# Kernel tuning notes

Measured on AMD Instinct MI355X. Metric: run time of the kernel, lower is better.

The kernel has to match this reference:

```python
import jax, jax.numpy as jnp
import numpy as np

T, H, E, K, I = 2048, 2048, 64, 8, 768
CAP = 512


def setup_inputs() -> dict:
    key = jax.random.key(0)
    ks = jax.random.split(key, 5)
    s = 0.02
    return {
        "hidden_states": jax.random.normal(ks[0], (T, H), jnp.float32),
        "w_router": jax.random.normal(ks[1], (E, H), jnp.float32) * s,
        "w_gate": jax.random.normal(ks[2], (E, H, I), jnp.float32) * s,
        "w_up": jax.random.normal(ks[3], (E, H, I), jnp.float32) * s,
        "w_down": jax.random.normal(ks[4], (E, I, H), jnp.float32) * s,
    }


def _moe(x, w_router, w_gate, w_up, w_down):
    Tn = x.shape[0]
    # --- router: softmax -> top-k -> renormalize (norm_topk_prob=True) ---
    logits = x @ w_router.T                                   # [T, E]
    probs = jax.nn.softmax(logits.astype(jnp.float32), axis=-1)
    topk_w, topk_idx = jax.lax.top_k(probs, K)                # [T, K]
    topk_w = topk_w / jnp.sum(topk_w, axis=-1, keepdims=True)
    # --- dispatch: sort (token, expert) pairs by expert, scatter into capacity buffers ---
    e = topk_idx.reshape(-1)                                  # [T*K] expert id per pair
    t = jnp.repeat(jnp.arange(Tn), K)                         # [T*K] token id per pair
    w = topk_w.reshape(-1)                                    # [T*K] combine weight per pair
    order = jnp.argsort(e, stable=True)
    e_s, t_s, w_s = e[order], t[order], w[order]
    counts = jax.ops.segment_sum(jnp.ones_like(e_s), e_s, num_segments=E)  # [E]
    starts = jnp.cumsum(counts) - counts                      # start offset of each expert group
    pos = jnp.arange(Tn * K) - starts[e_s]                    # slot within expert
    valid = pos < CAP
    posc = jnp.where(valid, pos, 0)
    vm = valid.astype(x.dtype)[:, None]
    buf = jnp.zeros((E, CAP, H), x.dtype).at[e_s, posc].add(x[t_s] * vm)   # [E, C, H]
    # --- grouped expert SwiGLU FFN: down(silu(gate(x)) * up(x)) ---
    g = jnp.einsum('ech,ehi->eci', buf, w_gate)               # [E, C, I]
    u = jnp.einsum('ech,ehi->eci', buf, w_up)                 # [E, C, I]
    y = jnp.einsum('eci,eih->ech', jax.nn.silu(g) * u, w_down)  # [E, C, H]
    # --- combine: gather expert outputs back to tokens, weighted sum ---
    gw = (w_s.astype(x.dtype) * valid.astype(x.dtype))[:, None]
    out = jnp.zeros((Tn, H), x.dtype).at[t_s].add(gw * y[e_s, posc])
    return out


def reference(hidden_states, w_router, w_gate, w_up, w_down):
    return _moe(hidden_states, w_router, w_gate, w_up, w_down)
```

## Files before the change

### kernel.cpp

```cpp
#include <hip/hip_runtime.h>
#include <hip/hip_bf16.h>
#include <math.h>

#define T_TOK 2048
#define H_DIM 2048
#define NEXP  64
#define TOPK  8
#define I_DIM 768
#define CAPE  512
#define MTMAX 4
#define LDW   40

typedef short bf16x8 __attribute__((ext_vector_type(8)));
typedef short bf16x4 __attribute__((ext_vector_type(4)));
typedef float f32x4  __attribute__((ext_vector_type(4)));

__device__ __forceinline__ unsigned short f2bf(float f) {
  unsigned u = __float_as_uint(f);
  u += 0x7fffu + ((u >> 16) & 1u);
  return (unsigned short)(u >> 16);
}
__device__ __forceinline__ float bf2f(unsigned short b) {
  return __uint_as_float(((unsigned)b) << 16);
}
__device__ __forceinline__ unsigned pack2(float lo, float hi) {
  return (unsigned)f2bf(lo) | ((unsigned)f2bf(hi) << 16);
}

__global__ __launch_bounds__(256) void k_router(const float* __restrict__ x,
                                                const float* __restrict__ wr,
                                                int* __restrict__ topk_idx,
                                                float* __restrict__ topk_w) {
  const int lane = threadIdx.x & 63;
  const int t = blockIdx.x * 4 + (threadIdx.x >> 6);
  const float4* xr   = (const float4*)(x + (size_t)t * H_DIM);
  const float4* wrow = (const float4*)(wr + (size_t)lane * H_DIM);
  double acc = 0.0;
  for (int i = 0; i < H_DIM / 4; ++i) {
    float4 a = xr[i], b = wrow[i];
    acc += (double)a.x * b.x; acc += (double)a.y * b.y;
    acc += (double)a.z * b.z; acc += (double)a.w * b.w;
  }
  float cur = (float)acc;
  float val[TOPK]; int idx[TOPK];
#pragma unroll
  for (int r = 0; r < TOPK; ++r) {
    float bv = cur; int bi = lane;
#pragma unroll
    for (int off = 32; off > 0; off >>= 1) {
      float ov = __shfl_xor(bv, off);
      int   oi = __shfl_xor(bi, off);
      if (ov > bv || (ov == bv && oi < bi)) { bv = ov; bi = oi; }
    }
    val[r] = bv; idx[r] = bi;
    if (lane == bi) cur = -INFINITY;
  }
  float m = val[0], s = 0.f, w[TOPK];
#pragma unroll
  for (int r = 0; r < TOPK; ++r) { w[r] = expf(val[r] - m); s += w[r]; }
  if (lane < TOPK) {
    topk_idx[t * TOPK + lane] = idx[lane];
    topk_w [t * TOPK + lane] = w[lane] / s;
  }
}

__global__ __launch_bounds__(256) void k_rank(const int* __restrict__ topk_idx,
                                              int* __restrict__ pair_pos,
                                              int* __restrict__ slot_token,
                                              int* __restrict__ cnts) {
  __shared__ int s_run[64];
  __shared__ int s_whist[4][64];
  const int tid = threadIdx.x, lane = tid & 63, wv = tid >> 6;
  if (tid < 64) s_run[tid] = 0;
  for (int c = 0; c < 64; ++c) {
    const int p = c * 256 + tid;
    const int e = topk_idx[p];
    __syncthreads();
    s_whist[wv][lane] = 0;
    __syncthreads();
    unsigned long long m = ~0ull;
#pragma unroll
    for (int b = 0; b < 6; ++b) {
      unsigned long long bb = __ballot((e >> b) & 1);
      m &= ((e >> b) & 1) ? bb : ~bb;
    }
    const int rw = __popcll(m & ((1ull << lane) - 1ull));
    if (rw == 0) s_whist[wv][e] = __popcll(m);
    __syncthreads();
    int r = rw;
    for (int w2 = 0; w2 < wv; ++w2) r += s_whist[w2][e];
    const int pos = s_run[e] + r;
    pair_pos[p] = pos;
    if (pos < CAPE) slot_token[e * CAPE + pos] = p >> 3;
    __syncthreads();
    if (tid < 64)
      s_run[tid] += s_whist[0][tid] + s_whist[1][tid] + s_whist[2][tid] + s_whist[3][tid];
  }
  __syncthreads();
  if (tid < 64) cnts[tid] = s_run[tid];
}

__global__ __launch_bounds__(512) void k_gateup(const float* __restrict__ x,
                                                const float* __restrict__ wg,
                                                const float* __restrict__ wu,
                                                const int* __restrict__ slot_token,
                                                const int* __restrict__ cnts,
                                                unsigned short* __restrict__ act) {
  const int NB = NEXP * MTMAX * 6;
  const int v = (blockIdx.x & 7) * (NB / 8) + (blockIdx.x >> 3);
  const int e = v / (MTMAX * 6);
  const int rem = v % (MTMAX * 6);
  const int mt = rem / 6, nt = rem % 6;

  int cnt = cnts[e]; cnt = cnt < CAPE ? cnt : CAPE;
  if (cnt <= 0 || mt * 128 >= cnt) return;
  const int m0 = mt << 7;

  __shared__ __align__(16) short As[2][128 * LDW];
  __shared__ __align__(16) short Bg[2][128 * LDW];
  __shared__ __align__(16) short Bu[2][128 * LDW];

  const int tid = threadIdx.x;
  const int lane = tid & 63, wave = tid >> 6;
  const int wm = wave >> 2, wn = wave & 3;
  const int lr = lane & 15, lg = lane >> 4;

  const int a_row0 = tid >> 3, a_kq = tid & 7;
  const int a_row1 = a_row0 + 64;
  const int b_kp = tid & 15, b_nq = tid >> 4;
  const int bk = 2 * b_kp, bn = 4 * b_nq;
  const size_t wbase = (size_t)e * H_DIM * I_DIM + (size_t)nt * 128;

  const int tok0 = (m0 + a_row0 < cnt) ? slot_token[e * CAPE + m0 + a_row0] : 0;
  const int tok1 = (m0 + a_row1 < cnt) ? slot_token[e * CAPE + m0 + a_row1] : 0;
  const float* xr0 = x + (size_t)tok0 * H_DIM + a_kq * 4;
  const float* xr1 = x + (size_t)tok1 * H_DIM + a_kq * 4;
  const float* gp  = wg + wbase + (size_t)bk * I_DIM + bn;
  const float* up  = wu + wbase + (size_t)bk * I_DIM + bn;

  f32x4 accg[4][2], accu[4][2];
#pragma unroll
  for (int mi = 0; mi < 4; ++mi)
#pragma unroll
    for (int ni = 0; ni < 2; ++ni) {
      accg[mi][ni] = (f32x4){0.f, 0.f, 0.f, 0.f};
      accu[mi][ni] = (f32x4){0.f, 0.f, 0.f, 0.f};
    }

  struct Tile { float4 a0, a1, g0, g1, u0, u1; };

  auto LOAD = [&](Tile& Tl, int kt) {
    const int k0 = kt * 32;
    Tl.a0 = *(const float4*)(xr0 + k0);
    Tl.a1 = *(const float4*)(xr1 + k0);
    Tl.g0 = *(const float4*)(gp + (size_t)k0 * I_DIM);
    Tl.g1 = *(const float4*)(gp + (size_t)k0 * I_DIM + I_DIM);
    Tl.u0 = *(const float4*)(up + (size_t)k0 * I_DIM);
    Tl.u1 = *(const float4*)(up + (size_t)k0 * I_DIM + I_DIM);
  };
  auto STORE = [&](const Tile& Tl, int b) {
    bf16x4 s0, s1;
    s0[0]=(short)f2bf(Tl.a0.x); s0[1]=(short)f2bf(Tl.a0.y); s0[2]=(short)f2bf(Tl.a0.z); s0[3]=(short)f2bf(Tl.a0.w);
    s1[0]=(short)f2bf(Tl.a1.x); s1[1]=(short)f2bf(Tl.a1.y); s1[2]=(short)f2bf(Tl.a1.z); s1[3]=(short)f2bf(Tl.a1.w);
    *(bf16x4*)(&As[b][a_row0 * LDW + a_kq * 4]) = s0;
    *(bf16x4*)(&As[b][a_row1 * LDW + a_kq * 4]) = s1;
    *(unsigned*)(&Bg[b][(bn + 0) * LDW + bk]) = pack2(Tl.g0.x, Tl.g1.x);
    *(unsigned*)(&Bg[b][(bn + 1) * LDW + bk]) = pack2(Tl.g0.y, Tl.g1.y);
    *(unsigned*)(&Bg[b][(bn + 2) * LDW + bk]) = pack2(Tl.g0.z, Tl.g1.z);
    *(unsigned*)(&Bg[b][(bn + 3) * LDW + bk]) = pack2(Tl.g0.w, Tl.g1.w);
    *(unsigned*)(&Bu[b][(bn + 0) * LDW + bk]) = pack2(Tl.u0.x, Tl.u1.x);
    *(unsigned*)(&Bu[b][(bn + 1) * LDW + bk]) = pack2(Tl.u0.y, Tl.u1.y);
    *(unsigned*)(&Bu[b][(bn + 2) * LDW + bk]) = pack2(Tl.u0.z, Tl.u1.z);
    *(unsigned*)(&Bu[b][(bn + 3) * LDW + bk]) = pack2(Tl.u0.w, Tl.u1.w);
  };
  auto COMPUTE = [&](int b) {
    bf16x8 a[4], bg[2], bu[2];
#pragma unroll
    for (int mi = 0; mi < 4; ++mi)
      a[mi] = *(const bf16x8*)(&As[b][(wm * 64 + mi * 16 + lr) * LDW + lg * 8]);
#pragma unroll
    for (int ni = 0; ni < 2; ++ni) {
      bg[ni] = *(const bf16x8*)(&Bg[b][(wn * 32 + ni * 16 + lr) * LDW + lg * 8]);
      bu[ni] = *(const bf16x8*)(&Bu[b][(wn * 32 + ni * 16 + lr) * LDW + lg * 8]);
    }
#pragma unroll
    for (int mi = 0; mi < 4; ++mi)
#pragma unroll
      for (int ni = 0; ni < 2; ++ni) {
        accg[mi][ni] = __builtin_amdgcn_mfma_f32_16x16x32_bf16(a[mi], bg[ni], accg[mi][ni], 0, 0, 0);
        accu[mi][ni] = __builtin_amdgcn_mfma_f32_16x16x32_bf16(a[mi], bu[ni], accu[mi][ni], 0, 0, 0);
      }
  };

  const int NK = H_DIM / 32;
  Tile tA, tB;
  LOAD(tA, 0);
  STORE(tA, 0);
  LOAD(tB, 1);
  __syncthreads();

  int t = 0;
#pragma unroll 1
  for (; t + 2 < NK; t += 2) {
    LOAD(tA, t + 2);
    COMPUTE(0);
    STORE(tB, 1);
    __syncthreads();
    LOAD(tB, t + 3);
    COMPUTE(1);
    STORE(tA, 0);
    __syncthreads();
  }
  COMPUTE(0);
  STORE(tB, 1);
  __syncthreads();
  COMPUTE(1);

#pragma unroll
  for (int mi = 0; mi < 4; ++mi)
#pragma unroll
    for (int ni = 0; ni < 2; ++ni)
#pragma unroll
      for (int r = 0; r < 4; ++r) {
        const int row = m0 + wm * 64 + mi * 16 + lg * 4 + r;
        const int col = nt * 128 + wn * 32 + ni * 16 + lr;
        const float g = accg[mi][ni][r], u = accu[mi][ni][r];
        const float vv = (g / (1.f + __expf(-g))) * u;
        act[(size_t)(e * CAPE + row) * I_DIM + col] = f2bf(vv);
      }
}

__global__ __launch_bounds__(512) void k_down(const unsigned short* __restrict__ act,
                                              const float* __restrict__ wd,
                                              const int* __restrict__ cnts,
                                              unsigned short* __restrict__ y) {
  const int NB = NEXP * MTMAX * 16;
  const int v = (blockIdx.x & 7) * (NB / 8) + (blockIdx.x >> 3);
  const int e = v / (MTMAX * 16);
  const int rem = v % (MTMAX * 16);
  const int mt = rem / 16, nt = rem % 16;

  int cnt = cnts[e]; cnt = cnt < CAPE ? cnt : CAPE;
  if (cnt <= 0 || mt * 128 >= cnt) return;
  const int m0 = mt << 7;

  __shared__ __align__(16) short As[2][128 * LDW];
  __shared__ __align__(16) short Bt[2][128 * LDW];

  const int tid = threadIdx.x;
  const int lane = tid & 63, wave = tid >> 6;
  const int wm = wave >> 2, wn = wave & 3;
  const int lr = lane & 15, lg = lane >> 4;

  const int a_row = tid >> 2, a_ko = (tid & 3) * 8;
  const int b_kp = tid & 15, b_nq = tid >> 4;
  const int bk = 2 * b_kp, bn = 4 * b_nq;
  const size_t wbase = (size_t)e * I_DIM * H_DIM + (size_t)nt * 128;

  const unsigned short* ap = act + (size_t)(e * CAPE + m0 + a_row) * I_DIM + a_ko;
  const float* dp = wd + wbase + (size_t)bk * H_DIM + bn;

  f32x4 acc[4][2];
#pragma unroll
  for (int mi = 0; mi < 4; ++mi)
#pragma unroll
    for (int ni = 0; ni < 2; ++ni) acc[mi][ni] = (f32x4){0.f, 0.f, 0.f, 0.f};

  struct Tile { bf16x8 a; float4 d0, d1; };

  auto LOAD = [&](Tile& Tl, int kt) {
    const int k0 = kt * 32;
    Tl.a  = *(const bf16x8*)(ap + k0);
    Tl.d0 = *(const float4*)(dp + (size_t)k0 * H_DIM);
    Tl.d1 = *(const float4*)(dp + (size_t)k0 * H_DIM + H_DIM);
  };
  auto STORE = [&](const Tile& Tl, int b) {
    *(bf16x8*)(&As[b][a_row * LDW + a_ko]) = Tl.a;
    *(unsigned*)(&Bt[b][(bn + 0) * LDW + bk]) = pack2(Tl.d0.x, Tl.d1.x);
    *(unsigned*)(&Bt[b][(bn + 1) * LDW + bk]) = pack2(Tl.d0.y, Tl.d1.y);
    *(unsigned*)(&Bt[b][(bn + 2) * LDW + bk]) = pack2(Tl.d0.z, Tl.d1.z);
    *(unsigned*)(&Bt[b][(bn + 3) * LDW + bk]) = pack2(Tl.d0.w, Tl.d1.w);
  };
  auto COMPUTE = [&](int b) {
    bf16x8 a[4], bb[2];
#pragma unroll
    for (int mi = 0; mi < 4; ++mi)
      a[mi] = *(const bf16x8*)(&As[b][(wm * 64 + mi * 16 + lr) * LDW + lg * 8]);
#pragma unroll
    for (int ni = 0; ni < 2; ++ni)
      bb[ni] = *(const bf16x8*)(&Bt[b][(wn * 32 + ni * 16 + lr) * LDW + lg * 8]);
#pragma unroll
    for (int mi = 0; mi < 4; ++mi)
#pragma unroll
      for (int ni = 0; ni < 2; ++ni)
        acc[mi][ni] = __builtin_amdgcn_mfma_f32_16x16x32_bf16(a[mi], bb[ni], acc[mi][ni], 0, 0, 0);
  };

  const int NK = I_DIM / 32;
  Tile tA, tB;
  LOAD(tA, 0);
  STORE(tA, 0);
  LOAD(tB, 1);
  __syncthreads();

  int t = 0;
#pragma unroll 1
  for (; t + 2 < NK; t += 2) {
    LOAD(tA, t + 2);
    COMPUTE(0);
    STORE(tB, 1);
    __syncthreads();
    LOAD(tB, t + 3);
    COMPUTE(1);
    STORE(tA, 0);
    __syncthreads();
  }
  COMPUTE(0);
  STORE(tB, 1);
  __syncthreads();
  COMPUTE(1);

#pragma unroll
  for (int mi = 0; mi < 4; ++mi)
#pragma unroll
    for (int ni = 0; ni < 2; ++ni)
#pragma unroll
      for (int r = 0; r < 4; ++r) {
        const int row = m0 + wm * 64 + mi * 16 + lg * 4 + r;
        const int col = nt * 128 + wn * 32 + ni * 16 + lr;
        y[(size_t)(e * CAPE + row) * H_DIM + col] = f2bf(acc[mi][ni][r]);
      }
}

__global__ __launch_bounds__(256) void k_combine(const unsigned short* __restrict__ y,
                                                 const int* __restrict__ topk_idx,
                                                 const float* __restrict__ topk_w,
                                                 const int* __restrict__ pair_pos,
                                                 float* __restrict__ out) {
  const int t = blockIdx.x;
  __shared__ int s_e[TOPK]; __shared__ int s_p[TOPK]; __shared__ float s_w[TOPK];
  if (threadIdx.x < TOPK) {
    s_e[threadIdx.x] = topk_idx[t * TOPK + threadIdx.x];
    s_p[threadIdx.x] = pair_pos[t * TOPK + threadIdx.x];
    s_w[threadIdx.x] = topk_w [t * TOPK + threadIdx.x];
  }
  __syncthreads();
  const int h0 = threadIdx.x * 8;
  float acc[8] = {0.f, 0.f, 0.f, 0.f, 0.f, 0.f, 0.f, 0.f};
#pragma unroll
  for (int k = 0; k < TOPK; ++k) {
    const int pos = s_p[k];
    if (pos >= CAPE) continue;
    const float w = s_w[k];
    const bf16x8 vv = *(const bf16x8*)(&y[(size_t)(s_e[k] * CAPE + pos) * H_DIM + h0]);
#pragma unroll
    for (int j = 0; j < 8; ++j) acc[j] += w * bf2f((unsigned short)vv[j]);
  }
  float4 o0 = {acc[0], acc[1], acc[2], acc[3]};
  float4 o1 = {acc[4], acc[5], acc[6], acc[7]};
  *(float4*)(out + (size_t)t * H_DIM + h0)     = o0;
  *(float4*)(out + (size_t)t * H_DIM + h0 + 4) = o1;
}

extern "C" void kernel_launch(void* const* d_in, const int* in_sizes, int n_in,
                              void* d_out, int out_size, void* d_ws, size_t ws_size,
                              hipStream_t stream) {
  const float* x   = (const float*)d_in[0];
  const float* wr  = (const float*)d_in[1];
  const float* wgt = (const float*)d_in[2];
  const float* wup = (const float*)d_in[3];
  const float* wdn = (const float*)d_in[4];
  float* out = (float*)d_out;

  char* ws = (char*)d_ws;
  int*            topk_idx   = (int*)(ws);
  float*          topk_w     = (float*)(ws + 65536);
  int*            pair_pos   = (int*)(ws + 131072);
  int*            cnts       = (int*)(ws + 196608);
  int*            slot_token = (int*)(ws + 196864);
  unsigned short* act        = (unsigned short*)(ws + 327936);
  unsigned short* yb         = (unsigned short*)(ws + 327936 + 50331648);

  k_router <<<dim3(T_TOK / 4),        dim3(256), 0, stream>>>(x, wr, topk_idx, topk_w);
  k_rank   <<<dim3(1),                dim3(256), 0, stream>>>(topk_idx, pair_pos, slot_token, cnts);
  k_gateup <<<dim3(NEXP * MTMAX * 6), dim3(512), 0, stream>>>(x, wgt, wup, slot_token, cnts, act);
  k_down   <<<dim3(NEXP * MTMAX * 16),dim3(512), 0, stream>>>(act, wdn, cnts, yb);
  k_combine<<<dim3(T_TOK),            dim3(256), 0, stream>>>(yb, topk_idx, topk_w, pair_pos, out);
}
```

Before: 803.6 us.

## Fuse combine into down-projection epilogue with weighted atomic adds to output

The down-projection kernel now scales each output row by its routing weight and atomically adds it straight into the token's output row. This removes the bf16 intermediate y buffer and the separate combine kernel. The rank kernel now records per-slot weights, and the output is zeroed with a memset. The bf16 packing also switches to the hardware paired-conversion intrinsic. The cost is many fp32 atomics to global memory (8 per output element) and a summation order that is no longer deterministic.

```diff
diff --git a/kernel.cpp b/kernel.cpp
--- a/kernel.cpp
+++ b/kernel.cpp
@@ -24,7 +24,8 @@
   return __uint_as_float(((unsigned)b) << 16);
 }
 __device__ __forceinline__ unsigned pack2(float lo, float hi) {
-  return (unsigned)f2bf(lo) | ((unsigned)f2bf(hi) << 16);
+  __hip_bfloat162 h = __float22bfloat162_rn(make_float2(lo, hi));
+  unsigned r; __builtin_memcpy(&r, &h, 4); return r;
 }
 
 __global__ __launch_bounds__(256) void k_router(const float* __restrict__ x,
@@ -65,8 +66,9 @@
 }
 
 __global__ __launch_bounds__(256) void k_rank(const int* __restrict__ topk_idx,
-                                              int* __restrict__ pair_pos,
+                                              const float* __restrict__ topk_w,
                                               int* __restrict__ slot_token,
+                                              float* __restrict__ slot_w,
                                               int* __restrict__ cnts) {
   __shared__ int s_run[64];
   __shared__ int s_whist[4][64];
@@ -90,8 +92,10 @@
     int r = rw;
     for (int w2 = 0; w2 < wv; ++w2) r += s_whist[w2][e];
     const int pos = s_run[e] + r;
-    pair_pos[p] = pos;
-    if (pos < CAPE) slot_token[e * CAPE + pos] = p >> 3;
+    if (pos < CAPE) {
+      slot_token[e * CAPE + pos] = p >> 3;
+      slot_w   [e * CAPE + pos] = topk_w[p];
+    }
     __syncthreads();
     if (tid < 64)
       s_run[tid] += s_whist[0][tid] + s_whist[1][tid] + s_whist[2][tid] + s_whist[3][tid];
@@ -159,11 +163,10 @@
     Tl.u1 = *(const float4*)(up + (size_t)k0 * I_DIM + I_DIM);
   };
   auto STORE = [&](const Tile& Tl, int b) {
-    bf16x4 s0, s1;
-    s0[0]=(short)f2bf(Tl.a0.x); s0[1]=(short)f2bf(Tl.a0.y); s0[2]=(short)f2bf(Tl.a0.z); s0[3]=(short)f2bf(Tl.a0.w);
-    s1[0]=(short)f2bf(Tl.a1.x); s1[1]=(short)f2bf(Tl.a1.y); s1[2]=(short)f2bf(Tl.a1.z); s1[3]=(short)f2bf(Tl.a1.w);
-    *(bf16x4*)(&As[b][a_row0 * LDW + a_kq * 4]) = s0;
-    *(bf16x4*)(&As[b][a_row1 * LDW + a_kq * 4]) = s1;
+    uint2 sa0 = { pack2(Tl.a0.x, Tl.a0.y), pack2(Tl.a0.z, Tl.a0.w) };
+    uint2 sa1 = { pack2(Tl.a1.x, Tl.a1.y), pack2(Tl.a1.z, Tl.a1.w) };
+    *(uint2*)(&As[b][a_row0 * LDW + a_kq * 4]) = sa0;
+    *(uint2*)(&As[b][a_row1 * LDW + a_kq * 4]) = sa1;
     *(unsigned*)(&Bg[b][(bn + 0) * LDW + bk]) = pack2(Tl.g0.x, Tl.g1.x);
     *(unsigned*)(&Bg[b][(bn + 1) * LDW + bk]) = pack2(Tl.g0.y, Tl.g1.y);
     *(unsigned*)(&Bg[b][(bn + 2) * LDW + bk]) = pack2(Tl.g0.z, Tl.g1.z);
@@ -233,7 +236,9 @@
 __global__ __launch_bounds__(512) void k_down(const unsigned short* __restrict__ act,
                                               const float* __restrict__ wd,
                                               const int* __restrict__ cnts,
-                                              unsigned short* __restrict__ y) {
+                                              const int* __restrict__ slot_token,
+                                              const float* __restrict__ slot_w,
+                                              float* __restrict__ out) {
   const int NB = NEXP * MTMAX * 16;
   const int v = (blockIdx.x & 7) * (NB / 8) + (blockIdx.x >> 3);
   const int e = v / (MTMAX * 16);
@@ -321,45 +326,19 @@
   COMPUTE(1);
 
 #pragma unroll
-  for (int mi = 0; mi < 4; ++mi)
-#pragma unroll
-    for (int ni = 0; ni < 2; ++ni)
-#pragma unroll
-      for (int r = 0; r < 4; ++r) {
-        const int row = m0 + wm * 64 + mi * 16 + lg * 4 + r;
-        const int col = nt * 128 + wn * 32 + ni * 16 + lr;
-        y[(size_t)(e * CAPE + row) * H_DIM + col] = f2bf(acc[mi][ni][r]);
-      }
-}
-
-__global__ __launch_bounds__(256) void k_combine(const unsigned short* __restrict__ y,
-                                                 const int* __restrict__ topk_idx,
-                                                 const float* __restrict__ topk_w,
-                                                 const int* __restrict__ pair_pos,
-                                                 float* __restrict__ out) {
-  const int t = blockIdx.x;
-  __shared__ int s_e[TOPK]; __shared__ int s_p[TOPK]; __shared__ float s_w[TOPK];
-  if (threadIdx.x < TOPK) {
-    s_e[threadIdx.x] = topk_idx[t * TOPK + threadIdx.x];
-    s_p[threadIdx.x] = pair_pos[t * TOPK + threadIdx.x];
-    s_w[threadIdx.x] = topk_w [t * TOPK + threadIdx.x];
-  }
-  __syncthreads();
-  const int h0 = threadIdx.x * 8;
-  float acc[8] = {0.f, 0.f, 0.f, 0.f, 0.f, 0.f, 0.f, 0.f};
-#pragma unroll
-  for (int k = 0; k < TOPK; ++k) {
-    const int pos = s_p[k];
-    if (pos >= CAPE) continue;
-    const float w = s_w[k];
-    const bf16x8 vv = *(const bf16x8*)(&y[(size_t)(s_e[k] * CAPE + pos) * H_DIM + h0]);
-#pragma unroll
-    for (int j = 0; j < 8; ++j) acc[j] += w * bf2f((unsigned short)vv[j]);
-  }
-  float4 o0 = {acc[0], acc[1], acc[2], acc[3]};
-  float4 o1 = {acc[4], acc[5], acc[6], acc[7]};
-  *(float4*)(out + (size_t)t * H_DIM + h0)     = o0;
-  *(float4*)(out + (size_t)t * H_DIM + h0 + 4) = o1;
+  for (int mi = 0; mi < 4; ++mi) {
+#pragma unroll
+    for (int r = 0; r < 4; ++r) {
+      const int row = m0 + wm * 64 + mi * 16 + lg * 4 + r;
+      if (row >= cnt) continue;
+      const int tok = slot_token[e * CAPE + row];
+      const float w = slot_w[e * CAPE + row];
+      float* orow = out + (size_t)tok * H_DIM + nt * 128 + wn * 32 + lr;
+#pragma unroll
+      for (int ni = 0; ni < 2; ++ni)
+        unsafeAtomicAdd(orow + ni * 16, w * acc[mi][ni][r]);
+    }
+  }
 }
 
 extern "C" void kernel_launch(void* const* d_in, const int* in_sizes, int n_in,
@@ -375,15 +354,14 @@
   char* ws = (char*)d_ws;
   int*            topk_idx   = (int*)(ws);
   float*          topk_w     = (float*)(ws + 65536);
-  int*            pair_pos   = (int*)(ws + 131072);
-  int*            cnts       = (int*)(ws + 196608);
-  int*            slot_token = (int*)(ws + 196864);
-  unsigned short* act        = (unsigned short*)(ws + 327936);
-  unsigned short* yb         = (unsigned short*)(ws + 327936 + 50331648);
-
+  int*            cnts       = (int*)(ws + 131072);
+  int*            slot_token = (int*)(ws + 131584);
+  float*          slot_w     = (float*)(ws + 262656);
+  unsigned short* act        = (unsigned short*)(ws + 524288);
+
+  hipMemsetAsync(out, 0, (size_t)out_size * sizeof(float), stream);
   k_router <<<dim3(T_TOK / 4),        dim3(256), 0, stream>>>(x, wr, topk_idx, topk_w);
-  k_rank   <<<dim3(1),                dim3(256), 0, stream>>>(topk_idx, pair_pos, slot_token, cnts);
+  k_rank   <<<dim3(1),                dim3(256), 0, stream>>>(topk_idx, topk_w, slot_token, slot_w, cnts);
   k_gateup <<<dim3(NEXP * MTMAX * 6), dim3(512), 0, stream>>>(x, wgt, wup, slot_token, cnts, act);
-  k_down   <<<dim3(NEXP * MTMAX * 16),dim3(512), 0, stream>>>(act, wdn, cnts, yb);
-  k_combine<<<dim3(T_TOK),            dim3(256), 0, stream>>>(yb, topk_idx, topk_w, pair_pos, out);
-}
+  k_down   <<<dim3(NEXP * MTMAX * 16),dim3(512), 0, stream>>>(act, wdn, cnts, slot_token, slot_w, out);
+}
```

Measured after the change: 835.0 us. 1.04x slower.
